# Kernel optimization log

Hardware: AMD Instinct MI355X
Metric: run time of the kernel (lower is better)

## Reference

```python
import jax, jax.numpy as jnp
import numpy as np

B, N, M, D, H = 2, 256, 64, 768, 12
HD = D // H  # head dim 64


def setup_inputs() -> dict:
    key = jax.random.key(0)
    ks = jax.random.split(key, 8)
    s = 0.02
    return {
        "x": jax.random.normal(ks[0], (B, N, D), jnp.float32),
        "sim_embeddings": jax.random.normal(ks[1], (B, N, M, D), jnp.float32),
        "Wq": jax.random.normal(ks[2], (D, D), jnp.float32) * s,
        "bq": jnp.zeros((D,), jnp.float32),
        "Wkv": jax.random.normal(ks[3], (D, 2 * D), jnp.float32) * s,
        "bkv": jnp.zeros((2 * D,), jnp.float32),
        "Wp": jax.random.normal(ks[4], (D, D), jnp.float32) * s,
        "bp": jnp.zeros((D,), jnp.float32),
    }


def reference(x, sim_embeddings, Wq, bq, Wkv, bkv, Wp, bp):
    # x: (B,N,D); sim_embeddings: (B,N,M,D)
    b, n, d = x.shape
    m = sim_embeddings.shape[2]
    scale = HD ** -0.5

    q = (x @ Wq + bq).reshape(b, n, H, HD).transpose(0, 2, 1, 3)  # (B,H,N,hd)

    kv_x = x @ Wkv + bkv                       # (B,N,2D)
    k_x, v_x = jnp.split(kv_x, 2, axis=-1)
    k_x = k_x.reshape(b, n, H, HD).transpose(0, 2, 1, 3)  # (B,H,N,hd) shared-global K
    v_x = v_x.reshape(b, n, H, HD).transpose(0, 2, 1, 3)

    kv_s = sim_embeddings @ Wkv + bkv          # (B,N,M,2D)
    k_s, v_s = jnp.split(kv_s, 2, axis=-1)
    k_s = k_s.reshape(b, n, m, H, HD).transpose(0, 3, 1, 2, 4)  # (B,H,N,M,hd) per-query local K
    v_s = v_s.reshape(b, n, m, H, HD).transpose(0, 3, 1, 2, 4)

    # scores over concatenated [global N keys | local M keys] without expanding K to (B,N,N+M,D)
    sg = jnp.einsum('bhnd,bhkd->bhnk', q, k_x) * scale   # (B,H,N,N)
    sl = jnp.einsum('bhnd,bhnmd->bhnm', q, k_s) * scale  # (B,H,N,M)
    attn = jax.nn.softmax(jnp.concatenate([sg, sl], axis=-1), axis=-1)
    ag, al = attn[..., :n], attn[..., n:]

    out = (jnp.einsum('bhnk,bhkd->bhnd', ag, v_x)
           + jnp.einsum('bhnm,bhnmd->bhnd', al, v_s))   # (B,H,N,hd)
    out = out.transpose(0, 2, 1, 3).reshape(b, n, d)
    return out @ Wp + bp
```

## Files before the change

kernel.cpp:

```cpp
#include <hip/hip_runtime.h>
#include <stdint.h>

#define DEV_INLINE __device__ __forceinline__

typedef __bf16 bf16x8 __attribute__((ext_vector_type(8)));
typedef float f32x4 __attribute__((ext_vector_type(4)));

typedef const __attribute__((address_space(1))) void* gas_ptr;
typedef __attribute__((address_space(3))) void* las_ptr;

DEV_INLINE unsigned short f2bf(float f) {
    union { float f; unsigned u; } v; v.f = f;
    unsigned r = v.u + 0x7fffu + ((v.u >> 16) & 1u);
    return (unsigned short)(r >> 16);
}

DEV_INLINE void lds_barrier() {
    __builtin_amdgcn_sched_barrier(0);
    asm volatile("s_waitcnt lgkmcnt(0)" ::: "memory");
    __builtin_amdgcn_s_barrier();
    __builtin_amdgcn_sched_barrier(0);
}

__global__ __launch_bounds__(256)
void prep_cast_kernel(const float* __restrict__ x, unsigned short* __restrict__ xb,
                      const float* __restrict__ Wkv, unsigned short* __restrict__ wkvb,
                      const float* __restrict__ bq, const float* __restrict__ bkv,
                      float* __restrict__ bias1, float* __restrict__ zbuf) {
    int bid = blockIdx.x;
    if (bid < 1536) {
        const float* s; unsigned short* d; long i;
        if (bid < 384) { s = x;   d = xb;   i = (long)bid * 256 + threadIdx.x; }
        else           { s = Wkv; d = wkvb; i = (long)(bid - 384) * 256 + threadIdx.x; }
        float4 a = ((const float4*)s)[i];
        ushort4 o;
        o.x = f2bf(a.x); o.y = f2bf(a.y); o.z = f2bf(a.z); o.w = f2bf(a.w);
        ((ushort4*)d)[i] = o;
    } else {
        int i = (bid - 1536) * 256 + threadIdx.x;
        if (i < 768) bias1[i] = bq[i];
        else if (i < 2304) bias1[i] = bkv[i - 768];
        else zbuf[i - 2304] = 0.f;
    }
}

__global__ void transpose3_kernel(const float* __restrict__ Wq,
                                  const float* __restrict__ Wkv,
                                  const float* __restrict__ Wp,
                                  unsigned short* __restrict__ w1t,
                                  unsigned short* __restrict__ wpt) {
    __shared__ float tl[64][65];
    int bx = blockIdx.x;
    const float* src; unsigned short* dst; int C;
    if (bx < 12)      { src = Wq;  dst = w1t;              C = 768; }
    else if (bx < 36) { src = Wkv; dst = w1t + 768L * 768; C = 1536; bx -= 12; }
    else              { src = Wp;  dst = wpt;              C = 768; bx -= 36; }
    int c0 = bx * 64, r0 = blockIdx.y * 64;
    int tx = threadIdx.x, ty = threadIdx.y;
    #pragma unroll
    for (int i = 0; i < 64; i += 16)
        tl[ty + i][tx] = src[(long)(r0 + ty + i) * C + c0 + tx];
    __syncthreads();
    #pragma unroll
    for (int i = 0; i < 64; i += 16)
        dst[(long)(c0 + ty + i) * 768 + r0 + tx] = f2bf(tl[tx][ty + i]);
}

template <int WM, int WN, int WAVES_M, bool G1E>
DEV_INLINE void gemm_body(const unsigned short* A, int lda,
                          const unsigned short* BT, int ldb,
                          const unsigned short* A2, int lda2,
                          const unsigned short* B2, int ldb2, int K1,
                          const float* bias, void* Cout, int ldc, int K,
                          const float* cin, int OUT, long obase, long tm, long tn,
                          unsigned short* As, unsigned short* Bs,
                          float* g1_qf, unsigned short* g1_qb,
                          unsigned short* g1_kxb, unsigned short* g1_vxT) {
    constexpr int TR = WAVES_M * WM * 16;
    constexpr int TC = (4 / WAVES_M) * WN * 16;
    const int tid = threadIdx.x;
    const int w = tid >> 6, lane = tid & 63;
    const int lm = lane & 15, quad = lane >> 4;
    const int m_off = (w % WAVES_M) * WM * 16;
    const int n_off = (w / WAVES_M) * WN * 16;
    const int lrow8 = lane >> 3;
    const int lcol_sw = (((lane & 7) ^ lrow8) * 8);

    f32x4 acc[WM][WN];
    #pragma unroll
    for (int mi = 0; mi < WM; ++mi)
        #pragma unroll
        for (int ni = 0; ni < WN; ++ni) acc[mi][ni] = f32x4{0.f, 0.f, 0.f, 0.f};

    for (int k0 = 0; k0 < K; k0 += 64) {
        const unsigned short* Ab; const unsigned short* Bb;
        int la, lb, kc;
        if (k0 < K1) { Ab = A;  Bb = BT; la = lda;  lb = ldb;  kc = k0; }
        else         { Ab = A2; Bb = B2; la = lda2; lb = ldb2; kc = k0 - K1; }
        __syncthreads();
        #pragma unroll
        for (int i = 0; i < TR / 32; ++i) {
            int rr = w * (TR / 4) + i * 8;
            const unsigned short* ga = Ab + (tm + rr + lrow8) * la + kc + lcol_sw;
            __builtin_amdgcn_global_load_lds((gas_ptr)ga, (las_ptr)(As + rr * 64), 16, 0, 0);
        }
        #pragma unroll
        for (int i = 0; i < TC / 32; ++i) {
            int rr = w * (TC / 4) + i * 8;
            const unsigned short* gb = Bb + (tn + rr + lrow8) * lb + kc + lcol_sw;
            __builtin_amdgcn_global_load_lds((gas_ptr)gb, (las_ptr)(Bs + rr * 64), 16, 0, 0);
        }
        __syncthreads();
        #pragma unroll
        for (int kk = 0; kk < 2; ++kk) {
            bf16x8 af[WM], bfr[WN];
            #pragma unroll
            for (int mi = 0; mi < WM; ++mi) {
                int r = m_off + mi * 16 + lm;
                af[mi] = *(const bf16x8*)(As + r * 64 + (((kk * 4 + quad) ^ (r & 7)) * 8));
            }
            #pragma unroll
            for (int ni = 0; ni < WN; ++ni) {
                int r = n_off + ni * 16 + lm;
                bfr[ni] = *(const bf16x8*)(Bs + r * 64 + (((kk * 4 + quad) ^ (r & 7)) * 8));
            }
            #pragma unroll
            for (int mi = 0; mi < WM; ++mi)
                #pragma unroll
                for (int ni = 0; ni < WN; ++ni)
                    acc[mi][ni] = __builtin_amdgcn_mfma_f32_16x16x32_bf16(
                        af[mi], bfr[ni], acc[mi][ni], 0, 0, 0);
        }
    }

    #pragma unroll
    for (int mi = 0; mi < WM; ++mi) {
        #pragma unroll
        for (int ni = 0; ni < WN; ++ni) {
            long col = tn + n_off + ni * 16 + lm;
            float bv = bias[col];
            #pragma unroll
            for (int r = 0; r < 4; ++r) {
                long row = tm + m_off + mi * 16 + quad * 4 + r;
                float v = acc[mi][ni][r] + bv;
                if (G1E) {
                    if (col < 768) {
                        g1_qf[row * 768 + col] = v;
                        g1_qb[row * 768 + col] = f2bf(v);
                    } else if (col < 1536) {
                        g1_kxb[row * 768 + (col - 768)] = f2bf(v);
                    } else {
                        int j = (int)col - 1536, h = j >> 6, d = j & 63;
                        int bb = (int)row >> 8, nn = (int)row & 255;
                        g1_vxT[((long)(bb * 12 + h) * 64 + d) * 256 + nn] = f2bf(v);
                    }
                } else {
                    long idx = obase + row * ldc + col;
                    if (cin) v += cin[idx];
                    if (OUT == 0) ((float*)Cout)[idx] = v;
                    else ((unsigned short*)Cout)[idx] = f2bf(v);
                }
            }
        }
    }
}

template <int WM, int WN, int WAVES_M, bool G1E>
__global__ __launch_bounds__(256)
void gemm_bf16_kernel(const unsigned short* __restrict__ A, int lda,
                      const unsigned short* __restrict__ BT, int ldb,
                      const float* __restrict__ bias,
                      void* __restrict__ Cout, int ldc, int K,
                      const float* __restrict__ cin, int OUT,
                      long aZb, long aZh, long bZb, long bZh, long oZb, long oZh,
                      float* __restrict__ g1_qf, unsigned short* __restrict__ g1_qb,
                      unsigned short* __restrict__ g1_kxb,
                      unsigned short* __restrict__ g1_vxT) {
    constexpr int TR = WAVES_M * WM * 16;
    constexpr int TC = (4 / WAVES_M) * WN * 16;
    __shared__ unsigned short As[TR * 64];
    __shared__ unsigned short Bs[TC * 64];
    const int z = blockIdx.z, zb = z / 12, zh = z % 12;
    gemm_body<WM, WN, WAVES_M, G1E>(
        A + zb * aZb + zh * aZh, lda, BT + zb * bZb + zh * bZh, ldb,
        nullptr, 0, nullptr, 0, 1 << 30,
        bias, Cout, ldc, K, cin, OUT, zb * oZb + zh * oZh,
        (long)blockIdx.y * TR, (long)blockIdx.x * TC, As, Bs,
        g1_qf, g1_qb, g1_kxb, g1_vxT);
}

__global__ __launch_bounds__(256)
void gemm_qwsg_kernel(const unsigned short* __restrict__ qb,
                      const unsigned short* __restrict__ wkvb,
                      const unsigned short* __restrict__ kxb,
                      const float* __restrict__ zbuf,
                      unsigned short* __restrict__ qWb,
                      float* __restrict__ sgbuf) {
    __shared__ unsigned short As[64 * 64];
    __shared__ unsigned short Bs[64 * 64];
    int bid = blockIdx.x;
    if (bid < 1152) {
        int bx = bid % 12, by = (bid / 12) % 8, h = bid / 96;
        gemm_body<2, 2, 2, false>(
            qb + h * 64, 768, wkvb + h * 64, 1536,
            nullptr, 0, nullptr, 0, 1 << 30,
            zbuf, qWb, 768, 64, nullptr, 1, (long)h * 393216,
            (long)by * 64, (long)bx * 64, As, Bs,
            nullptr, nullptr, nullptr, nullptr);
    } else {
        int bid2 = bid - 1152;
        int bx = bid2 % 4, by = (bid2 / 4) % 4, z = bid2 / 16;
        int zb = z / 12, zh = z % 12;
        gemm_body<2, 2, 2, false>(
            qb + zb * 196608 + zh * 64, 768, kxb + zb * 196608 + zh * 64, 768,
            nullptr, 0, nullptr, 0, 1 << 30,
            zbuf, sgbuf, 256, 64, nullptr, 0,
            (long)zb * 786432 + (long)zh * 65536,
            (long)by * 64, (long)bx * 64, As, Bs,
            nullptr, nullptr, nullptr, nullptr);
    }
}

template <int WM, int WN, int WAVES_M>
__global__ __launch_bounds__(256)
void gemm_concat_kernel(const unsigned short* __restrict__ A, int lda, long aZb, long aZh,
                        const unsigned short* __restrict__ BT, int ldb, long bZb, long bZh,
                        const unsigned short* __restrict__ A2, int lda2, long a2Zb, long a2Zh,
                        const unsigned short* __restrict__ B2, int ldb2, long b2Zb, long b2Zh,
                        int K1, int K, const float* __restrict__ bias,
                        void* __restrict__ Cout, int ldc,
                        const float* __restrict__ cin, int OUT, long oZb, long oZh) {
    constexpr int TR = WAVES_M * WM * 16;
    constexpr int TC = (4 / WAVES_M) * WN * 16;
    __shared__ unsigned short As[TR * 64];
    __shared__ unsigned short Bs[TC * 64];
    const int z = blockIdx.z, zb = z / 12, zh = z % 12;
    gemm_body<WM, WN, WAVES_M, false>(
        A + zb * aZb + zh * aZh, lda, BT + zb * bZb + zh * bZh, ldb,
        A2 + zb * a2Zb + zh * a2Zh, lda2, B2 + zb * b2Zb + zh * b2Zh, ldb2, K1,
        bias, Cout, ldc, K, cin, OUT, zb * oZb + zh * oZh,
        (long)blockIdx.y * TR, (long)blockIdx.x * TC, As, Bs,
        nullptr, nullptr, nullptr, nullptr);
}

__global__ __launch_bounds__(256)
void attn_fused_kernel(const float* __restrict__ sim,
                       const unsigned short* __restrict__ qWb,
                       const float* __restrict__ qf,
                       const float* __restrict__ bkv,
                       const float* __restrict__ sgbuf,
                       unsigned short* __restrict__ agb,
                       float* __restrict__ outg0,
                       float* __restrict__ al_g) {
    __shared__ unsigned short qw_s[16 * 784];
    __shared__ unsigned short sim_s[2][64 * 64];
    __shared__ float q_l[768];
    __shared__ float slb_s[12];
    __shared__ float scl[12][68];

    const int t = threadIdx.x;
    const int lane = t & 63, w = t >> 6;
    const int lm = lane & 15, quad = lane >> 4;
    const int n = blockIdx.x, b = blockIdx.y;
    const int n_ = b * 256 + n;
    const float* simn = sim + (long)n_ * 49152;

    {
        const int h = t >> 4, c0 = t & 15;
        const unsigned short* src = qWb + ((long)h * 512 + n_) * 768;
        #pragma unroll
        for (int j = 0; j < 6; ++j) {
            int ch = c0 + 16 * j;
            *(bf16x8*)(qw_s + h * 784 + ch * 8) = *(const bf16x8*)(src + ch * 8);
        }
    }
    q_l[t] = qf[(long)n_ * 768 + t];
    q_l[t + 256] = qf[(long)n_ * 768 + t + 256];
    q_l[t + 512] = qf[(long)n_ * 768 + t + 512];

    const int r0 = t >> 3, q8 = t & 7, r1 = r0 + 32;
    float4 p0a, p0b, p1a, p1b;
    {
        const float* g0 = simn + r0 * 768 + q8 * 8;
        p0a = *(const float4*)g0; p0b = *(const float4*)(g0 + 4);
        const float* g1 = simn + r1 * 768 + q8 * 8;
        p1a = *(const float4*)g1; p1b = *(const float4*)(g1 + 4);
    }
    __syncthreads();
    if (t < 12) {
        float s = 0.f;
        #pragma unroll 8
        for (int d = 0; d < 64; ++d) s += q_l[t * 64 + d] * bkv[t * 64 + d];
        slb_s[t] = s;
    }

    f32x4 acc = {};
    #pragma unroll
    for (int c = 0; c < 12; ++c) {
        const int k0 = c * 64;
        unsigned short* buf = sim_s[c & 1];
        union { bf16x8 v; unsigned short u[8]; } pk;
        pk.u[0] = f2bf(p0a.x); pk.u[1] = f2bf(p0a.y);
        pk.u[2] = f2bf(p0a.z); pk.u[3] = f2bf(p0a.w);
        pk.u[4] = f2bf(p0b.x); pk.u[5] = f2bf(p0b.y);
        pk.u[6] = f2bf(p0b.z); pk.u[7] = f2bf(p0b.w);
        *(bf16x8*)(buf + r0 * 64 + ((q8 ^ (r0 & 7)) * 8)) = pk.v;
        pk.u[0] = f2bf(p1a.x); pk.u[1] = f2bf(p1a.y);
        pk.u[2] = f2bf(p1a.z); pk.u[3] = f2bf(p1a.w);
        pk.u[4] = f2bf(p1b.x); pk.u[5] = f2bf(p1b.y);
        pk.u[6] = f2bf(p1b.z); pk.u[7] = f2bf(p1b.w);
        *(bf16x8*)(buf + r1 * 64 + ((q8 ^ (r1 & 7)) * 8)) = pk.v;
        if (c < 11) {
            const float* g0 = simn + r0 * 768 + k0 + 64 + q8 * 8;
            p0a = *(const float4*)g0; p0b = *(const float4*)(g0 + 4);
            const float* g1 = simn + r1 * 768 + k0 + 64 + q8 * 8;
            p1a = *(const float4*)g1; p1b = *(const float4*)(g1 + 4);
        }
        lds_barrier();
        #pragma unroll
        for (int kk = 0; kk < 2; ++kk) {
            int r = w * 16 + lm;
            bf16x8 af = *(const bf16x8*)(buf + r * 64 + (((kk * 4 + quad) ^ (r & 7)) * 8));
            bf16x8 bfr = *(const bf16x8*)(qw_s + lm * 784 + k0 + kk * 32 + quad * 8);
            acc = __builtin_amdgcn_mfma_f32_16x16x32_bf16(af, bfr, acc, 0, 0, 0);
        }
    }
    if (lm < 12) {
        #pragma unroll
        for (int r = 0; r < 4; ++r)
            scl[lm][w * 16 + quad * 4 + r] = (acc[r] + slb_s[lm]) * 0.125f;
    }
    __syncthreads();

    #pragma unroll
    for (int i = 0; i < 3; ++i) {
        const int h = w * 3 + i;
        const float* sgr = sgbuf + (long)(b * 12 + h) * 65536 + (long)n * 256;
        float v0 = sgr[lane] * 0.125f, v1 = sgr[lane + 64] * 0.125f,
              v2 = sgr[lane + 128] * 0.125f, v3 = sgr[lane + 192] * 0.125f;
        float v4 = scl[h][lane];
        float mx = fmaxf(fmaxf(fmaxf(v0, v1), fmaxf(v2, v3)), v4);
        #pragma unroll
        for (int off = 32; off > 0; off >>= 1) mx = fmaxf(mx, __shfl_xor(mx, off));
        float e0 = __expf(v0 - mx), e1 = __expf(v1 - mx), e2 = __expf(v2 - mx),
              e3 = __expf(v3 - mx), e4 = __expf(v4 - mx);
        float s = e0 + e1 + e2 + e3 + e4;
        #pragma unroll
        for (int off = 32; off > 0; off >>= 1) s += __shfl_xor(s, off);
        float inv = __frcp_rn(s);
        unsigned short* agr = agb + (long)(b * 12 + h) * 65536 + (long)n * 256;
        agr[lane] = f2bf(e0 * inv); agr[lane + 64] = f2bf(e1 * inv);
        agr[lane + 128] = f2bf(e2 * inv); agr[lane + 192] = f2bf(e3 * inv);
        float al = e4 * inv;
        al_g[(long)n_ * 768 + h * 64 + lane] = al;
        float am = al;
        #pragma unroll
        for (int off = 32; off > 0; off >>= 1) am += __shfl_xor(am, off);
        outg0[(long)n_ * 768 + h * 64 + lane] = am * bkv[768 + h * 64 + lane];
    }
}

__global__ __launch_bounds__(256)
void simbar_kernel(const float* __restrict__ sim,
                   const float* __restrict__ al_g,
                   unsigned short* __restrict__ simbar) {
    __shared__ float al_l[768];
    const int t = threadIdx.x;
    const int n_ = blockIdx.x;
    const int c = blockIdx.y * 256 + t;
    const float* simn = sim + (long)n_ * 49152;
    al_l[t] = al_g[(long)n_ * 768 + t];
    al_l[t + 256] = al_g[(long)n_ * 768 + t + 256];
    al_l[t + 512] = al_g[(long)n_ * 768 + t + 512];
    __syncthreads();
    float a[12];
    #pragma unroll
    for (int h = 0; h < 12; ++h) a[h] = 0.f;
    #pragma unroll 4
    for (int m = 0; m < 64; ++m) {
        float s = simn[(long)m * 768 + c];
        #pragma unroll
        for (int h = 0; h < 12; ++h) a[h] += al_l[h * 64 + m] * s;
    }
    #pragma unroll
    for (int h = 0; h < 12; ++h)
        simbar[((long)h * 512 + n_) * 768 + c] = f2bf(a[h]);
}


extern "C" void kernel_launch(void* const* d_in, const int* in_sizes, int n_in,
                              void* d_out, int out_size, void* d_ws, size_t ws_size,
                              hipStream_t stream) {
    const float* x   = (const float*)d_in[0];
    const float* sim = (const float*)d_in[1];
    const float* Wq  = (const float*)d_in[2];
    const float* bq  = (const float*)d_in[3];
    const float* Wkv = (const float*)d_in[4];
    const float* bkv = (const float*)d_in[5];
    const float* Wp  = (const float*)d_in[6];
    const float* bp  = (const float*)d_in[7];
    float* out = (float*)d_out;

    char* ws = (char*)d_ws;
    size_t off = 0;
    auto alloc = [&](size_t bytes) {
        char* p = ws + off;
        off += (bytes + 255) & ~(size_t)255;
        return p;
    };
    unsigned short* xb     = (unsigned short*)alloc(512UL * 768 * 2);
    unsigned short* w1t    = (unsigned short*)alloc(2304UL * 768 * 2);
    unsigned short* wkvb   = (unsigned short*)alloc(768UL * 1536 * 2);
    unsigned short* wpt    = (unsigned short*)alloc(768UL * 768 * 2);
    float*          qf     = (float*)alloc(512UL * 768 * 4);
    unsigned short* qb     = (unsigned short*)alloc(512UL * 768 * 2);
    unsigned short* kxb    = (unsigned short*)alloc(512UL * 768 * 2);
    unsigned short* vxT    = (unsigned short*)alloc(24UL * 64 * 256 * 2);
    unsigned short* qWb    = (unsigned short*)alloc(16UL * 512 * 768 * 2);
    float*          sgbuf  = (float*)alloc(24UL * 65536 * 4);
    unsigned short* agb    = (unsigned short*)alloc(24UL * 65536 * 2);
    float*          outg0  = (float*)alloc(512UL * 768 * 4);
    float*          al_g   = (float*)alloc(512UL * 768 * 4);
    unsigned short* simbar = (unsigned short*)alloc(12UL * 512 * 768 * 2);
    unsigned short* attnb  = (unsigned short*)alloc(512UL * 768 * 2);
    float*          bias1  = (float*)alloc(2304UL * 4);
    float*          zbuf   = (float*)alloc(768UL * 4);

    prep_cast_kernel<<<1548, 256, 0, stream>>>(x, xb, Wkv, wkvb, bq, bkv, bias1, zbuf);
    transpose3_kernel<<<dim3(48, 12), dim3(64, 16), 0, stream>>>(Wq, Wkv, Wp, w1t, wpt);

    gemm_bf16_kernel<2, 2, 2, true><<<dim3(36, 8, 1), 256, 0, stream>>>(
        xb, 768, w1t, 768, bias1, nullptr, 768, 768, nullptr, 0,
        0, 0, 0, 0, 0, 0, qf, qb, kxb, vxT);

    gemm_qwsg_kernel<<<1536, 256, 0, stream>>>(qb, wkvb, kxb, zbuf, qWb, sgbuf);

    attn_fused_kernel<<<dim3(256, 2), 256, 0, stream>>>(
        sim, qWb, qf, bkv, sgbuf, agb, outg0, al_g);

    simbar_kernel<<<dim3(512, 3), 256, 0, stream>>>(sim, al_g, simbar);

    gemm_concat_kernel<1, 1, 2><<<dim3(2, 8, 24), 256, 0, stream>>>(
        simbar, 768, 196608, 393216,
        w1t + 1536L * 768, 768, 0, 49152,
        agb, 256, 786432, 65536,
        vxT, 256, 196608, 16384,
        768, 1024, zbuf, attnb, 768, outg0, 1, 196608, 64);

    gemm_bf16_kernel<1, 1, 2, false><<<dim3(24, 16, 1), 256, 0, stream>>>(
        attnb, 768, wpt, 768, bp, out, 768, 768, nullptr, 0,
        0, 0, 0, 0, 0, 0, nullptr, nullptr, nullptr, nullptr);
}
```

Before: 241.0 us.

## Double-buffer GEMM LDS tiles and fuse simbar reduction into attention kernel

```diff
diff --git a/kernel.cpp b/kernel.cpp
--- a/kernel.cpp
+++ b/kernel.cpp
@@ -10,11 +10,19 @@
 typedef __attribute__((address_space(3))) void* las_ptr;
 
 DEV_INLINE unsigned short f2bf(float f) {
-    union { float f; unsigned u; } v; v.f = f;
-    unsigned r = v.u + 0x7fffu + ((v.u >> 16) & 1u);
-    return (unsigned short)(r >> 16);
-}
-
+    union { __bf16 h; unsigned short u; } v;
+    v.h = (__bf16)f;
+    return v.u;
+}
+
+template <int N> DEV_INLINE void waitcnt_vm() {
+    asm volatile("s_waitcnt vmcnt(%0)" :: "n"(N) : "memory");
+}
+DEV_INLINE void hard_barrier() {
+    __builtin_amdgcn_sched_barrier(0);
+    __builtin_amdgcn_s_barrier();
+    __builtin_amdgcn_sched_barrier(0);
+}
 DEV_INLINE void lds_barrier() {
     __builtin_amdgcn_sched_barrier(0);
     asm volatile("s_waitcnt lgkmcnt(0)" ::: "memory");
@@ -78,6 +86,7 @@
                           unsigned short* g1_kxb, unsigned short* g1_vxT) {
     constexpr int TR = WAVES_M * WM * 16;
     constexpr int TC = (4 / WAVES_M) * WN * 16;
+    constexpr int NL = TR / 32 + TC / 32;
     const int tid = threadIdx.x;
     const int w = tid >> 6, lane = tid & 63;
     const int lm = lane & 15, quad = lane >> 4;
@@ -92,37 +101,52 @@
         #pragma unroll
         for (int ni = 0; ni < WN; ++ni) acc[mi][ni] = f32x4{0.f, 0.f, 0.f, 0.f};
 
-    for (int k0 = 0; k0 < K; k0 += 64) {
+    auto stage = [&](int k0, int pb) {
         const unsigned short* Ab; const unsigned short* Bb;
         int la, lb, kc;
         if (k0 < K1) { Ab = A;  Bb = BT; la = lda;  lb = ldb;  kc = k0; }
         else         { Ab = A2; Bb = B2; la = lda2; lb = ldb2; kc = k0 - K1; }
-        __syncthreads();
+        unsigned short* Asb = As + pb * (TR * 64);
+        unsigned short* Bsb = Bs + pb * (TC * 64);
         #pragma unroll
         for (int i = 0; i < TR / 32; ++i) {
             int rr = w * (TR / 4) + i * 8;
             const unsigned short* ga = Ab + (tm + rr + lrow8) * la + kc + lcol_sw;
-            __builtin_amdgcn_global_load_lds((gas_ptr)ga, (las_ptr)(As + rr * 64), 16, 0, 0);
+            __builtin_amdgcn_global_load_lds((gas_ptr)ga, (las_ptr)(Asb + rr * 64), 16, 0, 0);
         }
         #pragma unroll
         for (int i = 0; i < TC / 32; ++i) {
             int rr = w * (TC / 4) + i * 8;
             const unsigned short* gb = Bb + (tn + rr + lrow8) * lb + kc + lcol_sw;
-            __builtin_amdgcn_global_load_lds((gas_ptr)gb, (las_ptr)(Bs + rr * 64), 16, 0, 0);
-        }
-        __syncthreads();
+            __builtin_amdgcn_global_load_lds((gas_ptr)gb, (las_ptr)(Bsb + rr * 64), 16, 0, 0);
+        }
+    };
+
+    stage(0, 0);
+    const int nt = K >> 6;
+    for (int t = 0; t < nt; ++t) {
+        const int cur = t & 1;
+        if (t + 1 < nt) {
+            stage((t + 1) << 6, cur ^ 1);
+            waitcnt_vm<NL>();
+        } else {
+            waitcnt_vm<0>();
+        }
+        hard_barrier();
+        const unsigned short* Asb = As + cur * (TR * 64);
+        const unsigned short* Bsb = Bs + cur * (TC * 64);
         #pragma unroll
         for (int kk = 0; kk < 2; ++kk) {
             bf16x8 af[WM], bfr[WN];
             #pragma unroll
             for (int mi = 0; mi < WM; ++mi) {
                 int r = m_off + mi * 16 + lm;
-                af[mi] = *(const bf16x8*)(As + r * 64 + (((kk * 4 + quad) ^ (r & 7)) * 8));
+                af[mi] = *(const bf16x8*)(Asb + r * 64 + (((kk * 4 + quad) ^ (r & 7)) * 8));
             }
             #pragma unroll
             for (int ni = 0; ni < WN; ++ni) {
                 int r = n_off + ni * 16 + lm;
-                bfr[ni] = *(const bf16x8*)(Bs + r * 64 + (((kk * 4 + quad) ^ (r & 7)) * 8));
+                bfr[ni] = *(const bf16x8*)(Bsb + r * 64 + (((kk * 4 + quad) ^ (r & 7)) * 8));
             }
             #pragma unroll
             for (int mi = 0; mi < WM; ++mi)
@@ -131,6 +155,7 @@
                     acc[mi][ni] = __builtin_amdgcn_mfma_f32_16x16x32_bf16(
                         af[mi], bfr[ni], acc[mi][ni], 0, 0, 0);
         }
+        hard_barrier();
     }
 
     #pragma unroll
@@ -178,8 +203,8 @@
                       unsigned short* __restrict__ g1_vxT) {
     constexpr int TR = WAVES_M * WM * 16;
     constexpr int TC = (4 / WAVES_M) * WN * 16;
-    __shared__ unsigned short As[TR * 64];
-    __shared__ unsigned short Bs[TC * 64];
+    __shared__ unsigned short As[2 * TR * 64];
+    __shared__ unsigned short Bs[2 * TC * 64];
     const int z = blockIdx.z, zb = z / 12, zh = z % 12;
     gemm_body<WM, WN, WAVES_M, G1E>(
         A + zb * aZb + zh * aZh, lda, BT + zb * bZb + zh * bZh, ldb,
@@ -196,8 +221,8 @@
                       const float* __restrict__ zbuf,
                       unsigned short* __restrict__ qWb,
                       float* __restrict__ sgbuf) {
-    __shared__ unsigned short As[64 * 64];
-    __shared__ unsigned short Bs[64 * 64];
+    __shared__ unsigned short As[2 * 64 * 64];
+    __shared__ unsigned short Bs[2 * 64 * 64];
     int bid = blockIdx.x;
     if (bid < 1152) {
         int bx = bid % 12, by = (bid / 12) % 8, h = bid / 96;
@@ -232,8 +257,8 @@
                         const float* __restrict__ cin, int OUT, long oZb, long oZh) {
     constexpr int TR = WAVES_M * WM * 16;
     constexpr int TC = (4 / WAVES_M) * WN * 16;
-    __shared__ unsigned short As[TR * 64];
-    __shared__ unsigned short Bs[TC * 64];
+    __shared__ unsigned short As[2 * TR * 64];
+    __shared__ unsigned short Bs[2 * TC * 64];
     const int z = blockIdx.z, zb = z / 12, zh = z % 12;
     gemm_body<WM, WN, WAVES_M, false>(
         A + zb * aZb + zh * aZh, lda, BT + zb * bZb + zh * bZh, ldb,
@@ -243,7 +268,7 @@
         nullptr, nullptr, nullptr, nullptr);
 }
 
-__global__ __launch_bounds__(256)
+__global__ __launch_bounds__(512, 4)
 void attn_fused_kernel(const float* __restrict__ sim,
                        const unsigned short* __restrict__ qWb,
                        const float* __restrict__ qf,
@@ -251,39 +276,44 @@
                        const float* __restrict__ sgbuf,
                        unsigned short* __restrict__ agb,
                        float* __restrict__ outg0,
-                       float* __restrict__ al_g) {
-    __shared__ unsigned short qw_s[16 * 784];
-    __shared__ unsigned short sim_s[2][64 * 64];
+                       unsigned short* __restrict__ simbar) {
+    __shared__ unsigned short qw_s[12 * 784];
+    __shared__ unsigned short sim_s[2][2][64 * 64];
     __shared__ float q_l[768];
     __shared__ float slb_s[12];
-    __shared__ float scl[12][68];
+    __shared__ float scl[2][12][68];
+    __shared__ float al_s[12][64];
 
     const int t = threadIdx.x;
     const int lane = t & 63, w = t >> 6;
     const int lm = lane & 15, quad = lane >> 4;
+    const int g = w >> 2, wl = w & 3;
+    const int tg = t & 255;
     const int n = blockIdx.x, b = blockIdx.y;
     const int n_ = b * 256 + n;
     const float* simn = sim + (long)n_ * 49152;
 
     {
-        const int h = t >> 4, c0 = t & 15;
-        const unsigned short* src = qWb + ((long)h * 512 + n_) * 768;
-        #pragma unroll
-        for (int j = 0; j < 6; ++j) {
-            int ch = c0 + 16 * j;
-            *(bf16x8*)(qw_s + h * 784 + ch * 8) = *(const bf16x8*)(src + ch * 8);
+        const int h = t >> 5, c0 = t & 31;
+        if (h < 12) {
+            const unsigned short* src = qWb + ((long)h * 512 + n_) * 768;
+            #pragma unroll
+            for (int j = 0; j < 3; ++j) {
+                int ch = c0 + 32 * j;
+                *(bf16x8*)(qw_s + h * 784 + ch * 8) = *(const bf16x8*)(src + ch * 8);
+            }
         }
     }
     q_l[t] = qf[(long)n_ * 768 + t];
-    q_l[t + 256] = qf[(long)n_ * 768 + t + 256];
-    q_l[t + 512] = qf[(long)n_ * 768 + t + 512];
-
-    const int r0 = t >> 3, q8 = t & 7, r1 = r0 + 32;
+    if (t < 256) q_l[t + 512] = qf[(long)n_ * 768 + t + 512];
+
+    const int r0 = tg >> 3, q8 = tg & 7, r1 = r0 + 32;
+    const int kb = g * 6;
     float4 p0a, p0b, p1a, p1b;
     {
-        const float* g0 = simn + r0 * 768 + q8 * 8;
+        const float* g0 = simn + r0 * 768 + kb * 64 + q8 * 8;
         p0a = *(const float4*)g0; p0b = *(const float4*)(g0 + 4);
-        const float* g1 = simn + r1 * 768 + q8 * 8;
+        const float* g1 = simn + r1 * 768 + kb * 64 + q8 * 8;
         p1a = *(const float4*)g1; p1b = *(const float4*)(g1 + 4);
     }
     __syncthreads();
@@ -296,9 +326,9 @@
 
     f32x4 acc = {};
     #pragma unroll
-    for (int c = 0; c < 12; ++c) {
-        const int k0 = c * 64;
-        unsigned short* buf = sim_s[c & 1];
+    for (int cc = 0; cc < 6; ++cc) {
+        const int k0 = (kb + cc) * 64;
+        unsigned short* buf = sim_s[g][cc & 1];
         union { bf16x8 v; unsigned short u[8]; } pk;
         pk.u[0] = f2bf(p0a.x); pk.u[1] = f2bf(p0a.y);
         pk.u[2] = f2bf(p0a.z); pk.u[3] = f2bf(p0a.w);
@@ -310,7 +340,7 @@
         pk.u[4] = f2bf(p1b.x); pk.u[5] = f2bf(p1b.y);
         pk.u[6] = f2bf(p1b.z); pk.u[7] = f2bf(p1b.w);
         *(bf16x8*)(buf + r1 * 64 + ((q8 ^ (r1 & 7)) * 8)) = pk.v;
-        if (c < 11) {
+        if (cc < 5) {
             const float* g0 = simn + r0 * 768 + k0 + 64 + q8 * 8;
             p0a = *(const float4*)g0; p0b = *(const float4*)(g0 + 4);
             const float* g1 = simn + r1 * 768 + k0 + 64 + q8 * 8;
@@ -319,7 +349,7 @@
         lds_barrier();
         #pragma unroll
         for (int kk = 0; kk < 2; ++kk) {
-            int r = w * 16 + lm;
+            int r = wl * 16 + lm;
             bf16x8 af = *(const bf16x8*)(buf + r * 64 + (((kk * 4 + quad) ^ (r & 7)) * 8));
             bf16x8 bfr = *(const bf16x8*)(qw_s + lm * 784 + k0 + kk * 32 + quad * 8);
             acc = __builtin_amdgcn_mfma_f32_16x16x32_bf16(af, bfr, acc, 0, 0, 0);
@@ -328,63 +358,68 @@
     if (lm < 12) {
         #pragma unroll
         for (int r = 0; r < 4; ++r)
-            scl[lm][w * 16 + quad * 4 + r] = (acc[r] + slb_s[lm]) * 0.125f;
+            scl[g][lm][wl * 16 + quad * 4 + r] = acc[r];
     }
     __syncthreads();
 
-    #pragma unroll
-    for (int i = 0; i < 3; ++i) {
-        const int h = w * 3 + i;
-        const float* sgr = sgbuf + (long)(b * 12 + h) * 65536 + (long)n * 256;
-        float v0 = sgr[lane] * 0.125f, v1 = sgr[lane + 64] * 0.125f,
-              v2 = sgr[lane + 128] * 0.125f, v3 = sgr[lane + 192] * 0.125f;
-        float v4 = scl[h][lane];
-        float mx = fmaxf(fmaxf(fmaxf(v0, v1), fmaxf(v2, v3)), v4);
-        #pragma unroll
-        for (int off = 32; off > 0; off >>= 1) mx = fmaxf(mx, __shfl_xor(mx, off));
-        float e0 = __expf(v0 - mx), e1 = __expf(v1 - mx), e2 = __expf(v2 - mx),
-              e3 = __expf(v3 - mx), e4 = __expf(v4 - mx);
-        float s = e0 + e1 + e2 + e3 + e4;
-        #pragma unroll
-        for (int off = 32; off > 0; off >>= 1) s += __shfl_xor(s, off);
-        float inv = __frcp_rn(s);
-        unsigned short* agr = agb + (long)(b * 12 + h) * 65536 + (long)n * 256;
-        agr[lane] = f2bf(e0 * inv); agr[lane + 64] = f2bf(e1 * inv);
-        agr[lane + 128] = f2bf(e2 * inv); agr[lane + 192] = f2bf(e3 * inv);
-        float al = e4 * inv;
-        al_g[(long)n_ * 768 + h * 64 + lane] = al;
-        float am = al;
-        #pragma unroll
-        for (int off = 32; off > 0; off >>= 1) am += __shfl_xor(am, off);
-        outg0[(long)n_ * 768 + h * 64 + lane] = am * bkv[768 + h * 64 + lane];
-    }
-}
-
-__global__ __launch_bounds__(256)
-void simbar_kernel(const float* __restrict__ sim,
-                   const float* __restrict__ al_g,
-                   unsigned short* __restrict__ simbar) {
-    __shared__ float al_l[768];
-    const int t = threadIdx.x;
-    const int n_ = blockIdx.x;
-    const int c = blockIdx.y * 256 + t;
-    const float* simn = sim + (long)n_ * 49152;
-    al_l[t] = al_g[(long)n_ * 768 + t];
-    al_l[t + 256] = al_g[(long)n_ * 768 + t + 256];
-    al_l[t + 512] = al_g[(long)n_ * 768 + t + 512];
+    if (w < 6) {
+        #pragma unroll
+        for (int i = 0; i < 2; ++i) {
+            const int h = w * 2 + i;
+            const float* sgr = sgbuf + (long)(b * 12 + h) * 65536 + (long)n * 256;
+            float v0 = sgr[lane] * 0.125f, v1 = sgr[lane + 64] * 0.125f,
+                  v2 = sgr[lane + 128] * 0.125f, v3 = sgr[lane + 192] * 0.125f;
+            float v4 = (scl[0][h][lane] + scl[1][h][lane] + slb_s[h]) * 0.125f;
+            float mx = fmaxf(fmaxf(fmaxf(v0, v1), fmaxf(v2, v3)), v4);
+            #pragma unroll
+            for (int off = 32; off > 0; off >>= 1) mx = fmaxf(mx, __shfl_xor(mx, off));
+            float e0 = __expf(v0 - mx), e1 = __expf(v1 - mx), e2 = __expf(v2 - mx),
+                  e3 = __expf(v3 - mx), e4 = __expf(v4 - mx);
+            float s = e0 + e1 + e2 + e3 + e4;
+            #pragma unroll
+            for (int off = 32; off > 0; off >>= 1) s += __shfl_xor(s, off);
+            float inv = __frcp_rn(s);
+            unsigned short* agr = agb + (long)(b * 12 + h) * 65536 + (long)n * 256;
+            agr[lane] = f2bf(e0 * inv); agr[lane + 64] = f2bf(e1 * inv);
+            agr[lane + 128] = f2bf(e2 * inv); agr[lane + 192] = f2bf(e3 * inv);
+            float al = e4 * inv;
+            al_s[h][lane] = al;
+            float am = al;
+            #pragma unroll
+            for (int off = 32; off > 0; off >>= 1) am += __shfl_xor(am, off);
+            outg0[(long)n_ * 768 + h * 64 + lane] = am * bkv[768 + h * 64 + lane];
+        }
+    }
     __syncthreads();
-    float a[12];
-    #pragma unroll
-    for (int h = 0; h < 12; ++h) a[h] = 0.f;
-    #pragma unroll 4
-    for (int m = 0; m < 64; ++m) {
-        float s = simn[(long)m * 768 + c];
-        #pragma unroll
-        for (int h = 0; h < 12; ++h) a[h] += al_l[h * 64 + m] * s;
-    }
-    #pragma unroll
-    for (int h = 0; h < 12; ++h)
-        simbar[((long)h * 512 + n_) * 768 + c] = f2bf(a[h]);
+
+    {
+        float a[12];
+        #pragma unroll
+        for (int h = 0; h < 12; ++h) a[h] = 0.f;
+        #pragma unroll 4
+        for (int m = 0; m < 64; ++m) {
+            float s = simn[(long)m * 768 + t];
+            #pragma unroll
+            for (int h = 0; h < 12; ++h) a[h] += al_s[h][m] * s;
+        }
+        #pragma unroll
+        for (int h = 0; h < 12; ++h)
+            simbar[((long)h * 512 + n_) * 768 + t] = f2bf(a[h]);
+    }
+    if (w < 4) {
+        float a[12];
+        #pragma unroll
+        for (int h = 0; h < 12; ++h) a[h] = 0.f;
+        #pragma unroll 4
+        for (int m = 0; m < 64; ++m) {
+            float s = simn[(long)m * 768 + 512 + t];
+            #pragma unroll
+            for (int h = 0; h < 12; ++h) a[h] += al_s[h][m] * s;
+        }
+        #pragma unroll
+        for (int h = 0; h < 12; ++h)
+            simbar[((long)h * 512 + n_) * 768 + 512 + t] = f2bf(a[h]);
+    }
 }
 
 
@@ -416,11 +451,10 @@
     unsigned short* qb     = (unsigned short*)alloc(512UL * 768 * 2);
     unsigned short* kxb    = (unsigned short*)alloc(512UL * 768 * 2);
     unsigned short* vxT    = (unsigned short*)alloc(24UL * 64 * 256 * 2);
-    unsigned short* qWb    = (unsigned short*)alloc(16UL * 512 * 768 * 2);
+    unsigned short* qWb    = (unsigned short*)alloc(12UL * 512 * 768 * 2);
     float*          sgbuf  = (float*)alloc(24UL * 65536 * 4);
     unsigned short* agb    = (unsigned short*)alloc(24UL * 65536 * 2);
     float*          outg0  = (float*)alloc(512UL * 768 * 4);
-    float*          al_g   = (float*)alloc(512UL * 768 * 4);
     unsigned short* simbar = (unsigned short*)alloc(12UL * 512 * 768 * 2);
     unsigned short* attnb  = (unsigned short*)alloc(512UL * 768 * 2);
     float*          bias1  = (float*)alloc(2304UL * 4);
@@ -429,16 +463,14 @@
     prep_cast_kernel<<<1548, 256, 0, stream>>>(x, xb, Wkv, wkvb, bq, bkv, bias1, zbuf);
     transpose3_kernel<<<dim3(48, 12), dim3(64, 16), 0, stream>>>(Wq, Wkv, Wp, w1t, wpt);
 
-    gemm_bf16_kernel<2, 2, 2, true><<<dim3(36, 8, 1), 256, 0, stream>>>(
+    gemm_bf16_kernel<1, 2, 2, true><<<dim3(36, 16, 1), 256, 0, stream>>>(
         xb, 768, w1t, 768, bias1, nullptr, 768, 768, nullptr, 0,
         0, 0, 0, 0, 0, 0, qf, qb, kxb, vxT);
 
     gemm_qwsg_kernel<<<1536, 256, 0, stream>>>(qb, wkvb, kxb, zbuf, qWb, sgbuf);
 
-    attn_fused_kernel<<<dim3(256, 2), 256, 0, stream>>>(
-        sim, qWb, qf, bkv, sgbuf, agb, outg0, al_g);
-
-    simbar_kernel<<<dim3(512, 3), 256, 0, stream>>>(sim, al_g, simbar);
+    attn_fused_kernel<<<dim3(256, 2), 512, 0, stream>>>(
+        sim, qWb, qf, bkv, sgbuf, agb, outg0, simbar);
 
     gemm_concat_kernel<1, 1, 2><<<dim3(2, 8, 24), 256, 0, stream>>>(
         simbar, 768, 196608, 393216,
```

Measured after the change: 236.1 us. 1.02x faster.
